# Kernel optimization log

Hardware: AMD Instinct MI355X
Metric: run time of the kernel (lower is better)

## Reference

```python
import jax, jax.numpy as jnp
import numpy as np

H = 1024      # hidden_size
NH = 16       # num_attention_heads
HD = H // NH  # attention_head_size = 64
B, S = 2, 2048


def setup_inputs() -> dict:
    key = jax.random.key(0)
    ks = jax.random.split(key, 8)
    scale = 1.0 / np.sqrt(H)
    return {
        "hidden_states": jax.random.normal(ks[0], (B, S, H), dtype=jnp.float32),
        "attention_mask": jnp.zeros((B, 1, 1, S), dtype=jnp.float32),
        "Wq": jax.random.normal(ks[1], (H, H), dtype=jnp.float32) * scale,
        "bq": jax.random.normal(ks[2], (H,), dtype=jnp.float32) * 0.02,
        "Wk": jax.random.normal(ks[3], (H, H), dtype=jnp.float32) * scale,
        "bk": jax.random.normal(ks[4], (H,), dtype=jnp.float32) * 0.02,
        "Wv": jax.random.normal(ks[5], (H, H), dtype=jnp.float32) * scale,
        "bv": jax.random.normal(ks[6], (H,), dtype=jnp.float32) * 0.02,
    }


def _split_heads(x):
    # [B,S,H] -> [B,NH,S,HD]
    b, s, _ = x.shape
    return x.reshape(b, s, NH, HD).transpose(0, 2, 1, 3)


def reference(hidden_states, attention_mask, Wq, bq, Wk, bk, Wv, bv):
    q = _split_heads(hidden_states @ Wq.T + bq)  # [B,NH,S,HD]
    k = _split_heads(hidden_states @ Wk.T + bk)
    v = _split_heads(hidden_states @ Wv.T + bv)
    scores = jnp.einsum("bhqd,bhkd->bhqk", q, k) / np.sqrt(HD).astype(np.float32)
    scores = scores + attention_mask  # additive mask, broadcast over heads/queries
    weights = jax.nn.softmax(scores, axis=-1)  # dropout is identity in eval mode
    ctx = jnp.einsum("bhqk,bhkd->bhqd", weights, v)  # [B,NH,S,HD]
    return ctx.transpose(0, 2, 1, 3).reshape(hidden_states.shape[0], hidden_states.shape[1], H)
```

## Files before the change

kernel.cpp:

```cpp
#include <hip/hip_runtime.h>
#include <hip/hip_bf16.h>
#include <math.h>

#define HSZ   1024
#define NHEAD 16
#define HDIM  64
#define BATCH 2
#define SEQ   2048

#define LOG2E 1.4426950408889634f

typedef __attribute__((ext_vector_type(8))) short short8;
typedef __attribute__((ext_vector_type(4))) short short4_t;
typedef __attribute__((ext_vector_type(4))) float floatx4;

typedef __attribute__((address_space(1))) const unsigned int gu32;
typedef __attribute__((address_space(3))) unsigned int lu32;

__device__ __forceinline__ void g2lds16(const void* g, void* l) {
    __builtin_amdgcn_global_load_lds((gu32*)g, (lu32*)l, 16, 0, 0);
}

__device__ __forceinline__ short f2bf(float f) {
    union { float f; unsigned u; } v; v.f = f;
    unsigned r = (v.u + 0x7FFF + ((v.u >> 16) & 1)) >> 16;
    return (short)r;
}

__device__ __forceinline__ unsigned pk2(float a, float b) {
    __hip_bfloat162 h = __float22bfloat162_rn(make_float2(a, b));
    return *(unsigned*)&h;
}

__device__ __forceinline__ float ex2(float x) {
#if __has_builtin(__builtin_amdgcn_exp2f)
    return __builtin_amdgcn_exp2f(x);
#else
    return exp2f(x);
#endif
}

__global__ __launch_bounds__(256) void convert_kernel(
    const float4* __restrict__ X, const float4* __restrict__ Wq,
    const float4* __restrict__ Wk, const float4* __restrict__ Wv,
    const float4* __restrict__ Mask,
    short4_t* __restrict__ Xb, short4_t* __restrict__ Wb,
    float4* __restrict__ Mw)
{
    int idx = blockIdx.x * 256 + threadIdx.x;
    if (idx >= 1835008) {
        int t = idx - 1835008;
        float4 f = Mask[t];
        float4 o;
        o.x = f.x * LOG2E; o.y = f.y * LOG2E;
        o.z = f.z * LOG2E; o.w = f.w * LOG2E;
        Mw[t] = o;
        return;
    }
    const float4* src; short4_t* dst;
    if (idx < 1048576) { src = X + idx; dst = Xb + idx; }
    else {
        int t = idx - 1048576;
        int sel = t >> 18;
        int wi  = t & 0x3FFFF;
        src = (sel == 0 ? Wq : sel == 1 ? Wk : Wv) + wi;
        dst = Wb + (sel << 18) + wi;
    }
    float4 f = *src;
    short4_t o;
    o.x = f2bf(f.x); o.y = f2bf(f.y); o.z = f2bf(f.z); o.w = f2bf(f.w);
    *dst = o;
}

__global__ __launch_bounds__(256, 3) void qkv_mfma_kernel(
    const short* __restrict__ Xb, const short* __restrict__ Wb,
    const float* __restrict__ bq, const float* __restrict__ bk,
    const float* __restrict__ bv,
    short* __restrict__ qo, short* __restrict__ ko, short* __restrict__ vT)
{
    __shared__ short Sm[128 * 132];
    short* As = Sm;
    short* Bs = Sm + 8192;

    const int tid  = threadIdx.x;
    const int lane = tid & 63;
    const int w    = tid >> 6;
    const int l    = lane & 15, quad = lane >> 4;
    const int gM   = blockIdx.y * 128;
    const int gN   = blockIdx.x * 128;
    const int wm   = (w >> 1) * 64, wn = (w & 1) * 64;
    const int ci   = lane >> 3, pb = lane & 7;

    floatx4 acc[4][4] = {};

    for (int kt = 0; kt < HSZ / 64; ++kt) {
        const int k0 = kt * 64;
        __syncthreads();
        #pragma unroll
        for (int u = 0; u < 4; ++u) {
            int c  = w * 4 + u;
            int r  = c * 8 + ci;
            int lb = pb ^ (r & 7);
            g2lds16(Xb + (size_t)(gM + r) * HSZ + k0 + lb * 8, &As[c * 512]);
            g2lds16(Wb + (size_t)(gN + r) * HSZ + k0 + lb * 8, &Bs[c * 512]);
        }
        __syncthreads();
        #pragma unroll
        for (int kk = 0; kk < 2; ++kk) {
            short8 a[4], b[4];
            #pragma unroll
            for (int i = 0; i < 4; ++i) {
                int m = wm + i * 16 + l;
                a[i] = *(const short8*)&As[m * 64 + (((quad + kk * 4) ^ (m & 7)) << 3)];
                int n = wn + i * 16 + l;
                b[i] = *(const short8*)&Bs[n * 64 + (((quad + kk * 4) ^ (n & 7)) << 3)];
            }
            #pragma unroll
            for (int i = 0; i < 4; ++i)
                #pragma unroll
                for (int j = 0; j < 4; ++j)
                    acc[i][j] = __builtin_amdgcn_mfma_f32_16x16x32_bf16(
                        a[i], b[j], acc[i][j], 0, 0, 0);
        }
    }

    const int mat = gN >> 10;

    if (mat == 2) {
        __syncthreads();
        #pragma unroll
        for (int j = 0; j < 4; ++j) {
            int fl = wn + j * 16 + l;
            float bv_ = bv[(gN & 1023) + fl];
            #pragma unroll
            for (int i = 0; i < 4; ++i)
                #pragma unroll
                for (int r = 0; r < 4; ++r)
                    Sm[fl * 132 + wm + i * 16 + quad * 4 + r]
                        = f2bf(acc[i][j][r] + bv_);
        }
        __syncthreads();
        const int bb = gM >> 11, ss0 = gM & (SEQ - 1);
        #pragma unroll
        for (int it = 0; it < 16; ++it) {
            int f = (tid >> 5) + it * 8;
            int c = (tid & 31) * 4;
            short4_t val = *(const short4_t*)&Sm[f * 132 + c];
            int b = (c >> 2) & 15;
            int cp = (c & ~63) | ((((b & 8) | ((b & 3) << 1) | ((b >> 2) & 1))) << 2);
            int nft = (gN & 1023) + f;
            int head = nft >> 6, d = nft & 63;
            *(short4_t*)&vT[(((size_t)(bb * NHEAD + head)) * HDIM + d) * SEQ
                            + ss0 + cp] = val;
        }
        return;
    }

    const float* bias = (mat == 0) ? bq : bk;
    short* dst        = (mat == 0) ? qo : ko;
    const float qscale = (mat == 0) ? 0.125f * LOG2E : 1.0f;

    #pragma unroll
    for (int j = 0; j < 4; ++j) {
        int nft = (gN & 1023) + wn + j * 16 + l;
        float bv_ = bias[nft];
        int head = nft >> 6, d = nft & 63;
        #pragma unroll
        for (int i = 0; i < 4; ++i) {
            #pragma unroll
            for (int r = 0; r < 4; ++r) {
                int gr = gM + wm + i * 16 + quad * 4 + r;
                int bb = gr >> 11, ss = gr & (SEQ - 1);
                float val = (acc[i][j][r] + bv_) * qscale;
                dst[((((size_t)bb * NHEAD + head) * SEQ + ss) << 6) + d] = f2bf(val);
            }
        }
    }
}

__global__ __launch_bounds__(512, 4) void attn_kernel(
    const short* __restrict__ Qg, const short* __restrict__ Kg,
    const short* __restrict__ VTg, const float* __restrict__ maskw,
    float* __restrict__ out)
{
    __shared__ short Qs[128 * 64];
    __shared__ alignas(16) short Ks[2][64 * 64];
    __shared__ alignas(16) short Vt[2][64 * 64];

    const int tid  = threadIdx.x;
    const int lane = tid & 63;
    const int w    = tid >> 6;
    const int l    = lane & 15, quad = lane >> 4;
    const int idx  = blockIdx.x;
    const int bh   = idx & 31;
    const int qt   = idx >> 5;
    const int batch = bh >> 4, head = bh & 15;
    const int ci = lane >> 3, pb = lane & 7;

    const short* Qb = Qg + ((size_t)bh * SEQ + qt * 128) * HDIM;
    const short* Kb = Kg + (size_t)bh * SEQ * HDIM;
    const short* Vb = VTg + (size_t)bh * HDIM * SEQ;
    const float* mrow = maskw + (size_t)batch * SEQ;

    #pragma unroll
    for (int u = 0; u < 2; ++u) {
        int c = w * 2 + u;
        int r = c * 8 + ci;
        int lb = pb ^ (r & 7);
        g2lds16(Qb + (size_t)r * HDIM + lb * 8, &Qs[c * 512]);
    }
    {
        int c = w;
        int r = c * 8 + ci;
        int lb = pb ^ (r & 7);
        g2lds16(Kb + (size_t)r * HDIM + lb * 8, &Ks[0][c * 512]);
        g2lds16(Vb + (size_t)r * SEQ + lb * 8, &Vt[0][c * 512]);
    }
    __syncthreads();

    short8 aq[2];
    #pragma unroll
    for (int kk = 0; kk < 2; ++kk) {
        int m = w * 16 + l;
        aq[kk] = *(const short8*)&Qs[m * 64 + (((quad + kk * 4) ^ (m & 7)) << 3)];
    }

    floatx4 o[4] = {};
    float l_i = 0.f;

    for (int kt = 0; kt < SEQ / 64; ++kt) {
        const int cur = kt & 1, nxt = cur ^ 1;
        if (kt + 1 < SEQ / 64) {
            const int r0 = (kt + 1) * 64;
            int c = w;
            int r = c * 8 + ci;
            int lb = pb ^ (r & 7);
            g2lds16(Kb + (size_t)(r0 + r) * HDIM + lb * 8, &Ks[nxt][c * 512]);
            g2lds16(Vb + (size_t)r * SEQ + r0 + lb * 8, &Vt[nxt][c * 512]);
        }

        const float* mg = mrow + kt * 64;
        floatx4 s[4];
        #pragma unroll
        for (int m = 0; m < 4; ++m) {
            float4 mq = *(const float4*)&mg[m * 16 + quad * 4];
            floatx4 ini = {mq.x, mq.y, mq.z, mq.w};
            s[m] = ini;
        }
        #pragma unroll
        for (int kk = 0; kk < 2; ++kk) {
            short8 ak[4];
            #pragma unroll
            for (int m = 0; m < 4; ++m) {
                int kr = m * 16 + l;
                ak[m] = *(const short8*)&Ks[cur][kr * 64 + (((quad + kk * 4) ^ (kr & 7)) << 3)];
            }
            __builtin_amdgcn_s_setprio(1);
            #pragma unroll
            for (int m = 0; m < 4; ++m)
                s[m] = __builtin_amdgcn_mfma_f32_16x16x32_bf16(
                    ak[m], aq[kk], s[m], 0, 0, 0);
            __builtin_amdgcn_s_setprio(0);
        }

        {
            float rs = 0.f;
            #pragma unroll
            for (int m = 0; m < 4; ++m) {
                s[m][0] = ex2(s[m][0]);
                s[m][1] = ex2(s[m][1]);
                s[m][2] = ex2(s[m][2]);
                s[m][3] = ex2(s[m][3]);
                rs += (s[m][0] + s[m][1]) + (s[m][2] + s[m][3]);
            }
            l_i += rs;
        }

        #pragma unroll
        for (int kb = 0; kb < 2; ++kb) {
            short8 bvf[4];
            #pragma unroll
            for (int nd = 0; nd < 4; ++nd) {
                int d = nd * 16 + l;
                bvf[nd] = *(const short8*)&Vt[cur][d * 64 + (((kb * 4 + quad) ^ (d & 7)) << 3)];
            }
            short8 ap;
            {
                union { unsigned u[4]; short8 s8; } pu;
                pu.u[0] = pk2(s[2 * kb][0], s[2 * kb][1]);
                pu.u[1] = pk2(s[2 * kb][2], s[2 * kb][3]);
                pu.u[2] = pk2(s[2 * kb + 1][0], s[2 * kb + 1][1]);
                pu.u[3] = pk2(s[2 * kb + 1][2], s[2 * kb + 1][3]);
                ap = pu.s8;
            }
            __builtin_amdgcn_s_setprio(1);
            #pragma unroll
            for (int nd = 0; nd < 4; ++nd)
                o[nd] = __builtin_amdgcn_mfma_f32_16x16x32_bf16(
                    ap, bvf[nd], o[nd], 0, 0, 0);
            __builtin_amdgcn_s_setprio(0);
        }

        __syncthreads();
    }

    {
        float t = l_i;
        t += __shfl_xor(t, 16);
        t += __shfl_xor(t, 32);
        l_i = t;
    }
    #pragma unroll
    for (int r = 0; r < 4; ++r) {
        float inv = 1.0f / __shfl(l_i, (lane & 48) + quad * 4 + r);
        int qrow = qt * 128 + w * 16 + quad * 4 + r;
        #pragma unroll
        for (int nd = 0; nd < 4; ++nd)
            out[((size_t)batch * SEQ + qrow) * HSZ + head * HDIM + nd * 16 + l]
                = o[nd][r] * inv;
    }
}

extern "C" void kernel_launch(void* const* d_in, const int* in_sizes, int n_in,
                              void* d_out, int out_size, void* d_ws, size_t ws_size,
                              hipStream_t stream) {
    const float* hs   = (const float*)d_in[0];
    const float* mask = (const float*)d_in[1];
    const float* Wq   = (const float*)d_in[2];
    const float* bq   = (const float*)d_in[3];
    const float* Wk   = (const float*)d_in[4];
    const float* bk   = (const float*)d_in[5];
    const float* Wv   = (const float*)d_in[6];
    const float* bv   = (const float*)d_in[7];
    float* out = (float*)d_out;

    short* Xb = (short*)d_ws;
    short* Wb = Xb + 4194304;
    short* qb = Wb + 3145728;
    short* kb = qb + 4194304;
    short* vT = kb + 4194304;
    float* Mw = (float*)(vT + 4194304);

    convert_kernel<<<7172, 256, 0, stream>>>(
        (const float4*)hs, (const float4*)Wq, (const float4*)Wk, (const float4*)Wv,
        (const float4*)mask, (short4_t*)Xb, (short4_t*)Wb, (float4*)Mw);

    dim3 g2(3 * HSZ / 128, BATCH * SEQ / 128);
    qkv_mfma_kernel<<<g2, 256, 0, stream>>>(Xb, Wb, bq, bk, bv, qb, kb, vT);

    attn_kernel<<<512, 512, 0, stream>>>(qb, kb, vT, Mw, out);
}
```

Before: 160.5 us.

## Software-pipeline attention loop with triple-buffered K/V and staggered QK/PV phases

Rebuilds the attention main loop as a software pipeline. K and V tiles go into three LDS buffers, K is prefetched two tiles ahead and V one tile ahead, and the QK^T of the next tile is interleaved with the softmax-exp and PV of the current tile. Explicit vmcnt waits plus raw barriers replace the full __syncthreads so MFMA work overlaps the async loads. The mask row is staged into LDS once rather than read from global memory every tile. This costs more LDS (extra buffers plus an 8KB mask array), which could lower occupancy, and the hand-counted waitcnt logic is fragile.

```diff
diff --git a/kernel.cpp b/kernel.cpp
--- a/kernel.cpp
+++ b/kernel.cpp
@@ -184,8 +184,9 @@
     float* __restrict__ out)
 {
     __shared__ short Qs[128 * 64];
-    __shared__ alignas(16) short Ks[2][64 * 64];
-    __shared__ alignas(16) short Vt[2][64 * 64];
+    __shared__ alignas(16) short Kb3[3][64 * 64];
+    __shared__ alignas(16) short Vb3[3][64 * 64];
+    __shared__ alignas(16) float Mf[SEQ];
 
     const int tid  = threadIdx.x;
     const int lane = tid & 63;
@@ -198,8 +199,8 @@
     const int ci = lane >> 3, pb = lane & 7;
 
     const short* Qb = Qg + ((size_t)bh * SEQ + qt * 128) * HDIM;
-    const short* Kb = Kg + (size_t)bh * SEQ * HDIM;
-    const short* Vb = VTg + (size_t)bh * HDIM * SEQ;
+    const short* Kg_ = Kg + (size_t)bh * SEQ * HDIM;
+    const short* Vg_ = VTg + (size_t)bh * HDIM * SEQ;
     const float* mrow = maskw + (size_t)batch * SEQ;
 
     #pragma unroll
@@ -209,12 +210,15 @@
         int lb = pb ^ (r & 7);
         g2lds16(Qb + (size_t)r * HDIM + lb * 8, &Qs[c * 512]);
     }
+    g2lds16(mrow + w * 256 + lane * 4, &Mf[w * 256]);
     {
-        int c = w;
-        int r = c * 8 + ci;
+        int r = w * 8 + ci;
         int lb = pb ^ (r & 7);
-        g2lds16(Kb + (size_t)r * HDIM + lb * 8, &Ks[0][c * 512]);
-        g2lds16(Vb + (size_t)r * SEQ + lb * 8, &Vt[0][c * 512]);
+        g2lds16(Kg_ + (size_t)r * HDIM + lb * 8,          &Kb3[0][w * 512]);
+        g2lds16(Kg_ + (size_t)(64 + r) * HDIM + lb * 8,   &Kb3[1][w * 512]);
+        g2lds16(Kg_ + (size_t)(128 + r) * HDIM + lb * 8,  &Kb3[2][w * 512]);
+        g2lds16(Vg_ + (size_t)r * SEQ + lb * 8,           &Vb3[0][w * 512]);
+        g2lds16(Vg_ + (size_t)r * SEQ + 64 + lb * 8,      &Vb3[1][w * 512]);
     }
     __syncthreads();
 
@@ -227,20 +231,28 @@
 
     floatx4 o[4] = {};
     float l_i = 0.f;
-
-    for (int kt = 0; kt < SEQ / 64; ++kt) {
-        const int cur = kt & 1, nxt = cur ^ 1;
-        if (kt + 1 < SEQ / 64) {
-            const int r0 = (kt + 1) * 64;
-            int c = w;
-            int r = c * 8 + ci;
-            int lb = pb ^ (r & 7);
-            g2lds16(Kb + (size_t)(r0 + r) * HDIM + lb * 8, &Ks[nxt][c * 512]);
-            g2lds16(Vb + (size_t)r * SEQ + r0 + lb * 8, &Vt[nxt][c * 512]);
-        }
-
-        const float* mg = mrow + kt * 64;
-        floatx4 s[4];
+    floatx4 sA[4], sB[4];
+
+    const short* kR; const short* kP; short* kW;
+    const short* vR; const short* vP; short* vW;
+
+    auto DMAK = [&](int t) {
+        int r = w * 8 + ci;
+        int lb = pb ^ (r & 7);
+        g2lds16(Kg_ + (size_t)(t * 64 + r) * HDIM + lb * 8, kW + w * 512);
+    };
+    auto DMAV = [&](int t) {
+        int r = w * 8 + ci;
+        int lb = pb ^ (r & 7);
+        g2lds16(Vg_ + (size_t)r * SEQ + t * 64 + lb * 8, vW + w * 512);
+    };
+    auto ROT = [&]() {
+        const short* tk = kR; kR = kP; kP = kW; kW = (short*)tk;
+        const short* tv = vR; vR = vP; vP = vW; vW = (short*)tv;
+    };
+
+    auto QKT = [&](floatx4 (&s)[4], const short* kbuf, int u1) {
+        const float* mg = &Mf[u1 * 64];
         #pragma unroll
         for (int m = 0; m < 4; ++m) {
             float4 mq = *(const float4*)&mg[m * 16 + quad * 4];
@@ -253,7 +265,7 @@
             #pragma unroll
             for (int m = 0; m < 4; ++m) {
                 int kr = m * 16 + l;
-                ak[m] = *(const short8*)&Ks[cur][kr * 64 + (((quad + kk * 4) ^ (kr & 7)) << 3)];
+                ak[m] = *(const short8*)&kbuf[kr * 64 + (((quad + kk * 4) ^ (kr & 7)) << 3)];
             }
             __builtin_amdgcn_s_setprio(1);
             #pragma unroll
@@ -262,7 +274,9 @@
                     ak[m], aq[kk], s[m], 0, 0, 0);
             __builtin_amdgcn_s_setprio(0);
         }
-
+    };
+
+    auto SMPV = [&](floatx4 (&s)[4], const short* vbuf) {
         {
             float rs = 0.f;
             #pragma unroll
@@ -275,14 +289,13 @@
             }
             l_i += rs;
         }
-
         #pragma unroll
         for (int kb = 0; kb < 2; ++kb) {
             short8 bvf[4];
             #pragma unroll
             for (int nd = 0; nd < 4; ++nd) {
                 int d = nd * 16 + l;
-                bvf[nd] = *(const short8*)&Vt[cur][d * 64 + (((kb * 4 + quad) ^ (d & 7)) << 3)];
+                bvf[nd] = *(const short8*)&vbuf[d * 64 + (((kb * 4 + quad) ^ (d & 7)) << 3)];
             }
             short8 ap;
             {
@@ -300,9 +313,46 @@
                     ap, bvf[nd], o[nd], 0, 0, 0);
             __builtin_amdgcn_s_setprio(0);
         }
-
-        __syncthreads();
-    }
+    };
+
+    QKT(sA, &Kb3[0][0], 0);
+    __syncthreads();
+    kR = &Kb3[1][0]; kP = &Kb3[2][0]; kW = &Kb3[0][0];
+    vR = &Vb3[0][0]; vP = &Vb3[1][0]; vW = &Vb3[2][0];
+
+#define PHASE_BAR(N)                                        \
+    asm volatile("s_waitcnt vmcnt(" #N ")" ::: "memory");   \
+    __builtin_amdgcn_s_barrier();                           \
+    asm volatile("" ::: "memory");
+
+    for (int t = 0; t < 28; t += 2) {
+        DMAK(t + 3); DMAV(t + 2);
+        QKT(sB, kR, t + 1);
+        SMPV(sA, vR);
+        PHASE_BAR(2)
+        ROT();
+        DMAK(t + 4); DMAV(t + 3);
+        QKT(sA, kR, t + 2);
+        SMPV(sB, vR);
+        PHASE_BAR(2)
+        ROT();
+    }
+    DMAK(31); DMAV(30);
+    QKT(sB, kR, 29);
+    SMPV(sA, vR);
+    PHASE_BAR(2)
+    ROT();
+    DMAV(31);
+    QKT(sA, kR, 30);
+    SMPV(sB, vR);
+    PHASE_BAR(1)
+    ROT();
+    QKT(sB, kR, 31);
+    SMPV(sA, vR);
+    PHASE_BAR(0)
+    ROT();
+    SMPV(sB, vR);
+#undef PHASE_BAR
 
     {
         float t = l_i;
```

After: 156.0 us. 2.8% less time.
